# Optimization experiments

Measured on AMD Instinct MI355X. Metric: run time of the kernel, lower is better.

The kernel has to match this reference:

```python
import jax, jax.numpy as jnp
import numpy as np

SHAPES = ((92, 160), (46, 80), (23, 40), (12, 20))  # multi-scale (H, W) per level
B, NQ, C, M, P = 8, 900, 256, 8, 4
L = len(SHAPES)
D = C // M          # head dim = 32
S = sum(h * w for h, w in SHAPES)  # 19560 flattened keys
NC = 10
FFN = 1024


def setup_inputs() -> dict:
    key = jax.random.key(0)
    ks = jax.random.split(key, 16)
    f = lambda k, sh, s=0.02: jax.random.normal(k, sh, dtype=jnp.float32) * s
    return dict(
        query=jax.random.normal(ks[0], (B, NQ, C), dtype=jnp.float32),
        value=jax.random.normal(ks[1], (B, S, C), dtype=jnp.float32),
        ref_points=jax.random.uniform(ks[2], (B, NQ, 2), dtype=jnp.float32),
        w_value=f(ks[3], (C, C)), b_value=jnp.zeros((C,), jnp.float32),
        w_off=f(ks[4], (C, M * L * P * 2)), b_off=f(ks[5], (M * L * P * 2,), 0.5),
        w_attn=f(ks[6], (C, M * L * P)), b_attn=jnp.zeros((M * L * P,), jnp.float32),
        w_out=f(ks[7], (C, C)), b_out=jnp.zeros((C,), jnp.float32),
        ln1_w=jnp.ones((C,), jnp.float32), ln1_b=jnp.zeros((C,), jnp.float32),
        w_ffn1=f(ks[8], (C, FFN)), b_ffn1=jnp.zeros((FFN,), jnp.float32),
        w_ffn2=f(ks[9], (FFN, C)), b_ffn2=jnp.zeros((C,), jnp.float32),
        ln2_w=jnp.ones((C,), jnp.float32), ln2_b=jnp.zeros((C,), jnp.float32),
        w_cls=f(ks[10], (C, NC)), b_cls=jnp.zeros((NC,), jnp.float32),
    )


def _ln(x, w, b, eps=1e-6):
    u = x.mean(-1, keepdims=True)
    s = ((x - u) ** 2).mean(-1, keepdims=True)
    return (x - u) * jax.lax.rsqrt(s + eps) * w + b


def _sample_level(v_l, loc, Hl, Wl):
    # v_l: [B, Hl*Wl, M, D] level features; loc: [B, NQ, M, P, 2] normalized sampling locations.
    # Bilinear interpolation with zero padding (grid_sample align_corners=False convention).
    x = loc[..., 0] * Wl - 0.5
    y = loc[..., 1] * Hl - 0.5
    x0 = jnp.floor(x)
    y0 = jnp.floor(y)
    lx, ly = x - x0, y - y0
    vt = jnp.transpose(v_l, (0, 2, 1, 3))  # [B, M, S_l, D]

    def gather(xi, yi):
        valid = ((xi >= 0) & (xi < Wl) & (yi >= 0) & (yi < Hl)).astype(v_l.dtype)
        idx = (jnp.clip(yi, 0, Hl - 1) * Wl + jnp.clip(xi, 0, Wl - 1)).astype(jnp.int32)
        idx = jnp.transpose(idx, (0, 2, 1, 3)).reshape(B, M, NQ * P)
        g = jnp.take_along_axis(vt, idx[..., None], axis=2).reshape(B, M, NQ, P, D)
        return g * jnp.transpose(valid, (0, 2, 1, 3))[..., None]

    x0i, y0i = x0.astype(jnp.int32), y0.astype(jnp.int32)
    g00 = gather(x0i, y0i)
    g01 = gather(x0i + 1, y0i)
    g10 = gather(x0i, y0i + 1)
    g11 = gather(x0i + 1, y0i + 1)
    wx = jnp.transpose(lx, (0, 2, 1, 3))[..., None]
    wy = jnp.transpose(ly, (0, 2, 1, 3))[..., None]
    return g00 * (1 - wx) * (1 - wy) + g01 * wx * (1 - wy) + g10 * (1 - wx) * wy + g11 * wx * wy


def reference(query, value, ref_points, w_value, b_value, w_off, b_off, w_attn, b_attn,
              w_out, b_out, ln1_w, ln1_b, w_ffn1, b_ffn1, w_ffn2, b_ffn2, ln2_w, ln2_b,
              w_cls, b_cls):
    v = (value @ w_value + b_value).reshape(B, S, M, D)
    off = (query @ w_off + b_off).reshape(B, NQ, M, L, P, 2)
    attn = jax.nn.softmax((query @ w_attn + b_attn).reshape(B, NQ, M, L * P), axis=-1)
    attn = attn.reshape(B, NQ, M, L, P)
    norm = jnp.asarray([[w, h] for h, w in SHAPES], dtype=query.dtype)  # [L, 2] (W, H)
    loc = ref_points[:, :, None, None, None, :] + off / norm[None, None, None, :, None, :]

    out = jnp.zeros((B, M, NQ, D), dtype=query.dtype)
    start = 0
    for l, (Hl, Wl) in enumerate(SHAPES):
        v_l = jax.lax.dynamic_slice_in_dim(v, start, Hl * Wl, axis=1)
        samp = _sample_level(v_l, loc[:, :, :, l], Hl, Wl)          # [B, M, NQ, P, D]
        a = jnp.transpose(attn[:, :, :, l], (0, 2, 1, 3))[..., None]  # [B, M, NQ, P, 1]
        out = out + (samp * a).sum(3)
        start += Hl * Wl

    feat = jnp.transpose(out, (0, 2, 1, 3)).reshape(B, NQ, C) @ w_out + b_out
    x = _ln(query + feat, ln1_w, ln1_b)
    h = jax.nn.relu(x @ w_ffn1 + b_ffn1) @ w_ffn2 + b_ffn2
    x = _ln(x + h, ln2_w, ln2_b)
    return x @ w_cls + b_cls
```

## Files before the change

### kernel.cpp

```cpp
#include <hip/hip_runtime.h>
#include <cstddef>
#include <cstdint>

#define B_    8
#define NQ_   900
#define C_    256
#define M_    8
#define P_    4
#define L_    4
#define D_    32
#define S_    19560
#define NC_   10
#define FFN_  1024
#define RQ_   (B_ * NQ_)
#define RV_   (B_ * S_)

typedef __attribute__((ext_vector_type(8))) short bf8_t;
typedef __attribute__((ext_vector_type(8))) unsigned short us8_t;
typedef __attribute__((ext_vector_type(4))) float f4_t;
typedef unsigned short ushort_t;

__device__ __forceinline__ unsigned short f2bf(float x) {
    union { float f; unsigned u; } v; v.f = x;
    unsigned r = v.u + 0x7FFF + ((v.u >> 16) & 1);
    return (unsigned short)(r >> 16);
}
__device__ __forceinline__ float bfu2f(unsigned short u) {
    union { unsigned u; float f; } v; v.u = ((unsigned)u) << 16; return v.f;
}

__global__ __launch_bounds__(256) void prep_weights(
    const float* __restrict__ w_value, const float* __restrict__ w_off,
    const float* __restrict__ w_attn,  const float* __restrict__ w_out,
    const float* __restrict__ w_ffn1,  const float* __restrict__ w_ffn2,
    short* __restrict__ WvT, short* __restrict__ WoaT, short* __restrict__ WoutT,
    short* __restrict__ Wf1T, short* __restrict__ Wf2T)
{
    const int mat = blockIdx.z;
    int K, N; const float* src; short* dst;
    switch (mat) {
        case 0: K = 256;  N = 256;  src = w_value; dst = WvT;  break;
        case 1: K = 256;  N = 384;  src = nullptr; dst = WoaT; break;
        case 2: K = 256;  N = 256;  src = w_out;   dst = WoutT; break;
        case 3: K = 256;  N = 1024; src = w_ffn1;  dst = Wf1T; break;
        default:K = 1024; N = 256;  src = w_ffn2;  dst = Wf2T; break;
    }
    const int ntn = N >> 6;
    const int kt = blockIdx.x / ntn, nt = blockIdx.x % ntn;
    if (kt >= (K >> 6)) return;

    __shared__ float t[64][65];
    const int tx = threadIdx.x & 63;
    const int ty = threadIdx.x >> 6;
#pragma unroll
    for (int i = 0; i < 64; i += 4) {
        const int k = kt * 64 + i + ty;
        const int n = nt * 64 + tx;
        float v;
        if (mat == 1) v = (n < 256) ? w_off[(size_t)k * 256 + n]
                                    : w_attn[(size_t)k * 128 + (n - 256)];
        else          v = src[(size_t)k * N + n];
        t[i + ty][tx] = v;
    }
    __syncthreads();
#pragma unroll
    for (int i = 0; i < 64; i += 4) {
        const int n = nt * 64 + i + ty;
        const int k = kt * 64 + tx;
        dst[(size_t)n * K + k] = (short)f2bf(t[tx][i + ty]);
    }
}

__global__ __launch_bounds__(384) void prep_bias(
    const float* __restrict__ b_off, const float* __restrict__ b_attn,
    float* __restrict__ bias_cat)
{
    const int t = threadIdx.x;
    bias_cat[t] = (t < 256) ? b_off[t] : b_attn[t - 256];
}

template <int MODE, int BM>
__global__ __launch_bounds__(256) void gemm_mfma(
    const float* __restrict__ A, const short* __restrict__ WT,
    const float* __restrict__ bias, const float* __restrict__ res,
    float* __restrict__ out, int R, int N, int K)
{
    constexpr int NI  = BM / 32;
    constexpr int AIT = BM * 8 / 256;
    constexpr int ASB = BM * 128;
    constexpr int SMEM_BYTES = (MODE == 1) ? (128 * 136 * 2) : (ASB + 16384);

    __shared__ __align__(16) char smem[SMEM_BYTES];
    short* As = (short*)smem;
    short* Bs = (short*)(smem + ASB);

    const int tid  = threadIdx.x;
    const int lane = tid & 63;
    const int wave = tid >> 6;
    const int wr   = wave >> 1;
    const int wc   = wave & 1;
    const int g    = lane >> 4;
    const int fr   = lane & 15;

    const int row0 = blockIdx.x * BM;
    const int col0 = blockIdx.y * 128;

    const int r_base = tid >> 3;
    const int ku     = tid & 7;

    float4 rA[AIT][2];
#pragma unroll
    for (int it = 0; it < AIT; ++it) {
        rA[it][0] = make_float4(0.f, 0.f, 0.f, 0.f);
        rA[it][1] = make_float4(0.f, 0.f, 0.f, 0.f);
    }
    int4 rB[4];

    f4_t acc[NI][4] = {};

    auto LOAD = [&](int k0) {
#pragma unroll
        for (int it = 0; it < AIT; ++it) {
            const int grow = row0 + it * 32 + r_base;
            if (grow < R) {
                rA[it][0] = *(const float4*)(A + (size_t)grow * K + k0 + ku * 8);
                rA[it][1] = *(const float4*)(A + (size_t)grow * K + k0 + ku * 8 + 4);
            }
        }
#pragma unroll
        for (int it = 0; it < 4; ++it) {
            const int n = it * 32 + r_base;
            rB[it] = *(const int4*)(WT + (size_t)(col0 + n) * K + k0 + ku * 8);
        }
    };
    auto WRITE = [&]() {
#pragma unroll
        for (int it = 0; it < AIT; ++it) {
            const int r = it * 32 + r_base;
            const float va[8] = {rA[it][0].x, rA[it][0].y, rA[it][0].z, rA[it][0].w,
                                 rA[it][1].x, rA[it][1].y, rA[it][1].z, rA[it][1].w};
            bf8_t pk;
#pragma unroll
            for (int j = 0; j < 8; ++j) pk[j] = (short)f2bf(va[j]);
            *(bf8_t*)&As[r * 64 + (ku ^ (r & 7)) * 8] = pk;
        }
#pragma unroll
        for (int it = 0; it < 4; ++it) {
            const int n = it * 32 + r_base;
            *(int4*)&Bs[n * 64 + (ku ^ (n & 7)) * 8] = rB[it];
        }
    };

    LOAD(0);
    for (int k0 = 0; k0 < K; k0 += 64) {
        WRITE();
        __syncthreads();
        if (k0 + 64 < K) LOAD(k0 + 64);
#pragma unroll
        for (int c = 0; c < 2; ++c) {
            bf8_t fa[NI], fb[4];
#pragma unroll
            for (int i = 0; i < NI; ++i) {
                const int ar = wr * (BM / 2) + i * 16 + fr;
                fa[i] = *(const bf8_t*)&As[ar * 64 + ((c * 4 + g) ^ (ar & 7)) * 8];
            }
#pragma unroll
            for (int j = 0; j < 4; ++j) {
                const int br = wc * 64 + j * 16 + fr;
                fb[j] = *(const bf8_t*)&Bs[br * 64 + ((c * 4 + g) ^ (br & 7)) * 8];
            }
#pragma unroll
            for (int i = 0; i < NI; ++i)
#pragma unroll
                for (int j = 0; j < 4; ++j)
                    acc[i][j] = __builtin_amdgcn_mfma_f32_16x16x32_bf16(
                        fa[i], fb[j], acc[i][j], 0, 0, 0);
        }
        __syncthreads();
    }

    if (MODE == 1) {
        ushort_t* eps = (ushort_t*)smem;
        ushort_t* outv = (ushort_t*)out;
#pragma unroll
        for (int j = 0; j < 4; ++j) {
            const int col_l = wc * 64 + j * 16 + fr;
            const float bcol = bias[col0 + col_l];
#pragma unroll
            for (int i = 0; i < NI; ++i)
#pragma unroll
                for (int r = 0; r < 4; ++r) {
                    const int row_l = wr * 64 + i * 16 + g * 4 + r;
                    eps[row_l * 136 + col_l] = f2bf(acc[i][j][r] + bcol);
                }
        }
        __syncthreads();
#pragma unroll
        for (int u = 0; u < 8; ++u) {
            const int unit = u * 256 + tid;
            const int sl = unit >> 4;
            const int cc = unit & 15;
            const int grow = row0 + sl;
            if (grow < R) {
                const int b = grow / S_;
                const int s = grow - b * S_;
                const int col = col0 + cc * 8;
                const int m = col >> 5;
                const int d = col & 31;
                const int4 w = *(const int4*)&eps[sl * 136 + cc * 8];
                *(int4*)&outv[(((size_t)(b * M_ + m)) * S_ + s) * D_ + d] = w;
            }
        }
    } else {
#pragma unroll
        for (int j = 0; j < 4; ++j) {
            const int col = col0 + wc * 64 + j * 16 + fr;
            const float bcol = bias[col];
#pragma unroll
            for (int i = 0; i < NI; ++i) {
#pragma unroll
                for (int r = 0; r < 4; ++r) {
                    const int row = row0 + wr * (BM / 2) + i * 16 + g * 4 + r;
                    if (row >= R) continue;
                    float vv = acc[i][j][r] + bcol;
                    if (MODE == 2) {
                        out[(size_t)row * N + col] = fmaxf(vv, 0.f);
                    } else if (MODE == 3) {
                        out[(size_t)row * N + col] = vv + res[(size_t)row * N + col];
                    } else {
                        out[(size_t)row * N + col] = vv;
                    }
                }
            }
        }
    }
}

__global__ __launch_bounds__(128) void softmax_loc_kernel(
    const float* __restrict__ oa, const float* __restrict__ ref,
    float* __restrict__ loc, float* __restrict__ attn)
{
    const int row = blockIdx.x;
    const int t   = threadIdx.x;
    const float Wtab[L_] = {160.f, 80.f, 40.f, 20.f};
    const float Htab[L_] = {92.f, 46.f, 23.f, 12.f};

    float vlog = oa[(size_t)row * 384 + 256 + t];
    float mx = vlog;
#pragma unroll
    for (int o = 8; o >= 1; o >>= 1) mx = fmaxf(mx, __shfl_xor(mx, o, 64));
    const float e = __expf(vlog - mx);
    float sm = e;
#pragma unroll
    for (int o = 8; o >= 1; o >>= 1) sm += __shfl_xor(sm, o, 64);
    attn[(size_t)row * 128 + t] = e / sm;

    const int m = t >> 4, l = (t >> 2) & 3, p = t & 3;
    const float rx = ref[(size_t)row * 2 + 0];
    const float ry = ref[(size_t)row * 2 + 1];
    const int oi = m * 32 + l * 8 + p * 2;
    loc[(size_t)row * 256 + oi + 0] = rx * Wtab[l] + oa[(size_t)row * 384 + oi + 0] - 0.5f;
    loc[(size_t)row * 256 + oi + 1] = ry * Htab[l] + oa[(size_t)row * 384 + oi + 1] - 0.5f;
}

__global__ __launch_bounds__(256) void sample_kernel(
    const ushort_t* __restrict__ v, const float* __restrict__ loc,
    const float* __restrict__ attn, float* __restrict__ outf)
{
    const int row0 = blockIdx.x * 8;
    const int t    = threadIdx.x;
    const int rl   = t >> 5;
    const int m    = (t >> 2) & 7;
    const int dg   = t & 3;

    __shared__ float sloc[8][8][33];
    __shared__ float satt[8][8][17];

    {
        const float4* src = (const float4*)(loc + (size_t)row0 * 256);
#pragma unroll
        for (int i = 0; i < 2; ++i) {
            const int u   = i * 256 + t;
            const int r_  = u >> 6;
            const int rem = u & 63;
            const int m_  = rem >> 3;
            const int c4  = (rem & 7) * 4;
            *(float4*)&sloc[r_][m_][c4] = src[u];
        }
        const float4* asrc = (const float4*)(attn + (size_t)row0 * 128);
        {
            const int u   = t;
            const int r_  = u >> 5;
            const int rem = u & 31;
            const int m_  = rem >> 2;
            const int c4  = (rem & 3) * 4;
            *(float4*)&satt[r_][m_][c4] = asrc[u];
        }
    }
    __syncthreads();

    const int row = row0 + rl;
    const int b   = row / NQ_;
    const ushort_t* vbase = v + (((size_t)(b * M_ + m)) * S_) * D_ + dg * 8;

    const int Wtab[L_] = {160, 80, 40, 20};
    const int Htab[L_] = {92, 46, 23, 12};
    const int Stab[L_] = {0, 14720, 18400, 19320};

    float acc[8] = {};

#pragma unroll
    for (int l = 0; l < L_; ++l) {
        const int Wl = Wtab[l], Hl = Htab[l], st = Stab[l];
#pragma unroll
        for (int p = 0; p < P_; ++p) {
            const float x = sloc[rl][m][l * 8 + p * 2 + 0];
            const float y = sloc[rl][m][l * 8 + p * 2 + 1];
            const float a = satt[rl][m][l * 4 + p];
            const float xf = floorf(x), yf = floorf(y);
            const int x0 = (int)xf, y0 = (int)yf;
            const float lx = x - xf, ly = y - yf;
            const float wx0 = (x0 >= 0 && x0 < Wl)         ? (1.f - lx) : 0.f;
            const float wx1 = (x0 + 1 >= 0 && x0 + 1 < Wl) ? lx         : 0.f;
            const float wy0 = (y0 >= 0 && y0 < Hl)         ? (1.f - ly) : 0.f;
            const float wy1 = (y0 + 1 >= 0 && y0 + 1 < Hl) ? ly         : 0.f;
            const float ay0 = a * wy0, ay1 = a * wy1;
            const float aw00 = ay0 * wx0, aw01 = ay0 * wx1;
            const float aw10 = ay1 * wx0, aw11 = ay1 * wx1;
            const int xc0 = min(max(x0, 0), Wl - 1);
            const int xc1 = min(max(x0 + 1, 0), Wl - 1);
            const int yc0 = min(max(y0, 0), Hl - 1);
            const int yc1 = min(max(y0 + 1, 0), Hl - 1);
            const us8_t s00 = *(const us8_t*)(vbase + (size_t)(st + yc0 * Wl + xc0) * D_);
            const us8_t s01 = *(const us8_t*)(vbase + (size_t)(st + yc0 * Wl + xc1) * D_);
            const us8_t s10 = *(const us8_t*)(vbase + (size_t)(st + yc1 * Wl + xc0) * D_);
            const us8_t s11 = *(const us8_t*)(vbase + (size_t)(st + yc1 * Wl + xc1) * D_);
#pragma unroll
            for (int j = 0; j < 8; ++j)
                acc[j] += aw00 * bfu2f(s00[j]) + aw01 * bfu2f(s01[j])
                        + aw10 * bfu2f(s10[j]) + aw11 * bfu2f(s11[j]);
        }
    }

    float* o = outf + (size_t)row * 256 + m * 32 + dg * 8;
    *(float4*)o       = make_float4(acc[0], acc[1], acc[2], acc[3]);
    *((float4*)o + 1) = make_float4(acc[4], acc[5], acc[6], acc[7]);
}

__global__ __launch_bounds__(64) void ln_kernel(
    const float* __restrict__ in, const float* __restrict__ w,
    const float* __restrict__ bp, float* __restrict__ out)
{
    const int row  = blockIdx.x;
    const int lane = threadIdx.x;
    const float4 x = ((const float4*)(in + (size_t)row * C_))[lane];
    float s = x.x + x.y + x.z + x.w;
#pragma unroll
    for (int o = 32; o >= 1; o >>= 1) s += __shfl_xor(s, o, 64);
    const float mean = s * (1.f / C_);
    const float d0 = x.x - mean, d1 = x.y - mean, d2 = x.z - mean, d3 = x.w - mean;
    float ss = d0 * d0 + d1 * d1 + d2 * d2 + d3 * d3;
#pragma unroll
    for (int o = 32; o >= 1; o >>= 1) ss += __shfl_xor(ss, o, 64);
    const float r = rsqrtf(ss * (1.f / C_) + 1e-6f);
    const float4 wv = ((const float4*)w)[lane];
    const float4 bv = ((const float4*)bp)[lane];
    float4 o4;
    o4.x = d0 * r * wv.x + bv.x;
    o4.y = d1 * r * wv.y + bv.y;
    o4.z = d2 * r * wv.z + bv.z;
    o4.w = d3 * r * wv.w + bv.w;
    ((float4*)(out + (size_t)row * C_))[lane] = o4;
}

__global__ __launch_bounds__(64) void cls_kernel(
    const float* __restrict__ x, const float* __restrict__ w,
    const float* __restrict__ bias, float* __restrict__ out)
{
    const int row  = blockIdx.x;
    const int lane = threadIdx.x;
    float acc[NC_] = {};
#pragma unroll
    for (int j = 0; j < 4; ++j) {
        const int k = lane + j * 64;
        const float xk = x[(size_t)row * C_ + k];
        const float* wr = w + (size_t)k * NC_;
#pragma unroll
        for (int n = 0; n < NC_; ++n) acc[n] += xk * wr[n];
    }
#pragma unroll
    for (int n = 0; n < NC_; ++n) {
        float s = acc[n];
#pragma unroll
        for (int o = 32; o >= 1; o >>= 1) s += __shfl_xor(s, o, 64);
        if (lane == n) out[(size_t)row * NC_ + n] = s + bias[n];
    }
}

extern "C" void kernel_launch(void* const* d_in, const int* in_sizes, int n_in,
                              void* d_out, int out_size, void* d_ws, size_t ws_size,
                              hipStream_t stream)
{
    const float* query   = (const float*)d_in[0];
    const float* value   = (const float*)d_in[1];
    const float* refp    = (const float*)d_in[2];
    const float* w_value = (const float*)d_in[3];
    const float* b_value = (const float*)d_in[4];
    const float* w_off   = (const float*)d_in[5];
    const float* b_off   = (const float*)d_in[6];
    const float* w_attn  = (const float*)d_in[7];
    const float* b_attn  = (const float*)d_in[8];
    const float* w_out   = (const float*)d_in[9];
    const float* b_out   = (const float*)d_in[10];
    const float* ln1w    = (const float*)d_in[11];
    const float* ln1b    = (const float*)d_in[12];
    const float* w_ffn1  = (const float*)d_in[13];
    const float* b_ffn1  = (const float*)d_in[14];
    const float* w_ffn2  = (const float*)d_in[15];
    const float* b_ffn2  = (const float*)d_in[16];
    const float* ln2w    = (const float*)d_in[17];
    const float* ln2b    = (const float*)d_in[18];
    const float* w_cls   = (const float*)d_in[19];
    const float* b_cls   = (const float*)d_in[20];

    short* WvT   = (short*)d_ws;
    short* WoaT  = WvT  + 65536;
    short* WoutT = WoaT + 98304;
    short* Wf1T  = WoutT + 65536;
    short* Wf2T  = Wf1T + 262144;
    float* bias_cat = (float*)(Wf2T + 262144);
    ushort_t* v = (ushort_t*)(bias_cat + 384);
    float* oa   = (float*)(v + (size_t)RV_ * C_);
    float* loc  = oa   + (size_t)RQ_ * 384;
    float* attn = loc  + (size_t)RQ_ * 256;
    float* feat = attn + (size_t)RQ_ * 128;
    float* tmp  = feat + (size_t)RQ_ * 256;
    float* h    = tmp  + (size_t)RQ_ * 256;
    float* x2   = h    + (size_t)RQ_ * FFN_;

    prep_weights<<<dim3(64, 1, 5), 256, 0, stream>>>(
        w_value, w_off, w_attn, w_out, w_ffn1, w_ffn2,
        WvT, WoaT, WoutT, Wf1T, Wf2T);
    prep_bias<<<1, 384, 0, stream>>>(b_off, b_attn, bias_cat);

    gemm_mfma<1, 128><<<dim3((RV_ + 127) / 128, 2), 256, 0, stream>>>(
        value, WvT, b_value, nullptr, (float*)v, RV_, 256, 256);

    gemm_mfma<0, 64><<<dim3((RQ_ + 63) / 64, 3), 256, 0, stream>>>(
        query, WoaT, bias_cat, nullptr, oa, RQ_, 384, 256);

    softmax_loc_kernel<<<RQ_, 128, 0, stream>>>(oa, refp, loc, attn);

    sample_kernel<<<RQ_ / 8, 256, 0, stream>>>(v, loc, attn, feat);

    gemm_mfma<3, 64><<<dim3((RQ_ + 63) / 64, 2), 256, 0, stream>>>(
        feat, WoutT, b_out, query, tmp, RQ_, 256, 256);

    ln_kernel<<<RQ_, 64, 0, stream>>>(tmp, ln1w, ln1b, feat);

    gemm_mfma<2, 64><<<dim3((RQ_ + 63) / 64, 8), 256, 0, stream>>>(
        feat, Wf1T, b_ffn1, nullptr, h, RQ_, 1024, 256);

    gemm_mfma<3, 64><<<dim3((RQ_ + 63) / 64, 2), 256, 0, stream>>>(
        h, Wf2T, b_ffn2, feat, tmp, RQ_, 256, 1024);

    ln_kernel<<<RQ_, 64, 0, stream>>>(tmp, ln2w, ln2b, x2);

    cls_kernel<<<RQ_, 64, 0, stream>>>(x2, w_cls, b_cls, (float*)d_out);
}
```

Baseline: 504.8 us.

## Add dedicated full-width value projection GEMM with 512 threads per block

Result: faster. 493.6 us (-2.2%).

```diff
diff --git a/kernel.cpp b/kernel.cpp
--- a/kernel.cpp
+++ b/kernel.cpp
@@ -79,6 +79,135 @@
     bias_cat[t] = (t < 256) ? b_off[t] : b_attn[t - 256];
 }
 
+__global__ __launch_bounds__(512, 4) void gemm_value(
+    const float* __restrict__ A, const short* __restrict__ WT,
+    const float* __restrict__ bias, ushort_t* __restrict__ outv, int R)
+{
+    __shared__ __align__(16) char smem[49152];
+    short* As = (short*)smem;
+    short* Bs = (short*)(smem + 16384);
+
+    const int tid  = threadIdx.x;
+    const int lane = tid & 63;
+    const int wave = tid >> 6;
+    const int wr   = wave >> 2;
+    const int wc   = wave & 3;
+    const int g    = lane >> 4;
+    const int fr   = lane & 15;
+
+    const int row0 = blockIdx.x * 128;
+
+    const int r_base = tid >> 3;
+    const int ku     = tid & 7;
+
+    float4 rA[2][2];
+#pragma unroll
+    for (int it = 0; it < 2; ++it) {
+        rA[it][0] = make_float4(0.f, 0.f, 0.f, 0.f);
+        rA[it][1] = make_float4(0.f, 0.f, 0.f, 0.f);
+    }
+    int4 rB[4];
+    f4_t acc[4][4] = {};
+
+    auto LOAD = [&](int k0) {
+#pragma unroll
+        for (int it = 0; it < 2; ++it) {
+            const int grow = row0 + it * 64 + r_base;
+            if (grow < R) {
+                rA[it][0] = *(const float4*)(A + (size_t)grow * 256 + k0 + ku * 8);
+                rA[it][1] = *(const float4*)(A + (size_t)grow * 256 + k0 + ku * 8 + 4);
+            }
+        }
+#pragma unroll
+        for (int it = 0; it < 4; ++it) {
+            const int n = it * 64 + r_base;
+            rB[it] = *(const int4*)(WT + (size_t)n * 256 + k0 + ku * 8);
+        }
+    };
+    auto WRITE = [&]() {
+#pragma unroll
+        for (int it = 0; it < 2; ++it) {
+            const int r = it * 64 + r_base;
+            const float va[8] = {rA[it][0].x, rA[it][0].y, rA[it][0].z, rA[it][0].w,
+                                 rA[it][1].x, rA[it][1].y, rA[it][1].z, rA[it][1].w};
+            bf8_t pk;
+#pragma unroll
+            for (int j = 0; j < 8; ++j) pk[j] = (short)f2bf(va[j]);
+            *(bf8_t*)&As[r * 64 + (ku ^ (r & 7)) * 8] = pk;
+        }
+#pragma unroll
+        for (int it = 0; it < 4; ++it) {
+            const int n = it * 64 + r_base;
+            *(int4*)&Bs[n * 64 + (ku ^ (n & 7)) * 8] = rB[it];
+        }
+    };
+
+    LOAD(0);
+    for (int k0 = 0; k0 < 256; k0 += 64) {
+        WRITE();
+        __syncthreads();
+        if (k0 + 64 < 256) LOAD(k0 + 64);
+#pragma unroll
+        for (int c = 0; c < 2; ++c) {
+            bf8_t fa[4], fb[4];
+#pragma unroll
+            for (int i = 0; i < 4; ++i) {
+                const int ar = wr * 64 + i * 16 + fr;
+                fa[i] = *(const bf8_t*)&As[ar * 64 + ((c * 4 + g) ^ (ar & 7)) * 8];
+            }
+#pragma unroll
+            for (int j = 0; j < 4; ++j) {
+                const int br = wc * 64 + j * 16 + fr;
+                fb[j] = *(const bf8_t*)&Bs[br * 64 + ((c * 4 + g) ^ (br & 7)) * 8];
+            }
+#pragma unroll
+            for (int i = 0; i < 4; ++i)
+#pragma unroll
+                for (int j = 0; j < 4; ++j)
+                    acc[i][j] = __builtin_amdgcn_mfma_f32_16x16x32_bf16(
+                        fa[i], fb[j], acc[i][j], 0, 0, 0);
+        }
+        __syncthreads();
+    }
+
+    ushort_t* eps = (ushort_t*)smem;
+    for (int h = 0; h < 2; ++h) {
+        __syncthreads();
+        if ((wc >> 1) == h) {
+            const int wcl = wc & 1;
+#pragma unroll
+            for (int j = 0; j < 4; ++j) {
+                const int col_l = wcl * 64 + j * 16 + fr;
+                const float bcol = bias[h * 128 + col_l];
+#pragma unroll
+                for (int i = 0; i < 4; ++i)
+#pragma unroll
+                    for (int r = 0; r < 4; ++r) {
+                        const int row_l = wr * 64 + i * 16 + g * 4 + r;
+                        eps[row_l * 136 + col_l] = f2bf(acc[i][j][r] + bcol);
+                    }
+            }
+        }
+        __syncthreads();
+#pragma unroll
+        for (int u = 0; u < 4; ++u) {
+            const int unit = u * 512 + tid;
+            const int sl = unit >> 4;
+            const int cc = unit & 15;
+            const int grow = row0 + sl;
+            if (grow < R) {
+                const int b = grow / S_;
+                const int s = grow - b * S_;
+                const int col = h * 128 + cc * 8;
+                const int m = col >> 5;
+                const int d = col & 31;
+                *(int4*)&outv[(((size_t)(b * M_ + m)) * S_ + s) * D_ + d] =
+                    *(const int4*)&eps[sl * 136 + cc * 8];
+            }
+        }
+    }
+}
+
 template <int MODE, int BM>
 __global__ __launch_bounds__(256) void gemm_mfma(
     const float* __restrict__ A, const short* __restrict__ WT,
@@ -88,7 +217,7 @@
     constexpr int NI  = BM / 32;
     constexpr int AIT = BM * 8 / 256;
     constexpr int ASB = BM * 128;
-    constexpr int SMEM_BYTES = (MODE == 1) ? (128 * 136 * 2) : (ASB + 16384);
+    constexpr int SMEM_BYTES = ASB + 16384;
 
     __shared__ __align__(16) char smem[SMEM_BYTES];
     short* As = (short*)smem;
@@ -179,57 +308,23 @@
         __syncthreads();
     }
 
-    if (MODE == 1) {
-        ushort_t* eps = (ushort_t*)smem;
-        ushort_t* outv = (ushort_t*)out;
-#pragma unroll
-        for (int j = 0; j < 4; ++j) {
-            const int col_l = wc * 64 + j * 16 + fr;
-            const float bcol = bias[col0 + col_l];
-#pragma unroll
-            for (int i = 0; i < NI; ++i)
-#pragma unroll
-                for (int r = 0; r < 4; ++r) {
-                    const int row_l = wr * 64 + i * 16 + g * 4 + r;
-                    eps[row_l * 136 + col_l] = f2bf(acc[i][j][r] + bcol);
-                }
-        }
-        __syncthreads();
-#pragma unroll
-        for (int u = 0; u < 8; ++u) {
-            const int unit = u * 256 + tid;
-            const int sl = unit >> 4;
-            const int cc = unit & 15;
-            const int grow = row0 + sl;
-            if (grow < R) {
-                const int b = grow / S_;
-                const int s = grow - b * S_;
-                const int col = col0 + cc * 8;
-                const int m = col >> 5;
-                const int d = col & 31;
-                const int4 w = *(const int4*)&eps[sl * 136 + cc * 8];
-                *(int4*)&outv[(((size_t)(b * M_ + m)) * S_ + s) * D_ + d] = w;
-            }
-        }
-    } else {
-#pragma unroll
-        for (int j = 0; j < 4; ++j) {
-            const int col = col0 + wc * 64 + j * 16 + fr;
-            const float bcol = bias[col];
-#pragma unroll
-            for (int i = 0; i < NI; ++i) {
-#pragma unroll
-                for (int r = 0; r < 4; ++r) {
-                    const int row = row0 + wr * (BM / 2) + i * 16 + g * 4 + r;
-                    if (row >= R) continue;
-                    float vv = acc[i][j][r] + bcol;
-                    if (MODE == 2) {
-                        out[(size_t)row * N + col] = fmaxf(vv, 0.f);
-                    } else if (MODE == 3) {
-                        out[(size_t)row * N + col] = vv + res[(size_t)row * N + col];
-                    } else {
-                        out[(size_t)row * N + col] = vv;
-                    }
+#pragma unroll
+    for (int j = 0; j < 4; ++j) {
+        const int col = col0 + wc * 64 + j * 16 + fr;
+        const float bcol = bias[col];
+#pragma unroll
+        for (int i = 0; i < NI; ++i) {
+#pragma unroll
+            for (int r = 0; r < 4; ++r) {
+                const int row = row0 + wr * (BM / 2) + i * 16 + g * 4 + r;
+                if (row >= R) continue;
+                float vv = acc[i][j][r] + bcol;
+                if (MODE == 2) {
+                    out[(size_t)row * N + col] = fmaxf(vv, 0.f);
+                } else if (MODE == 3) {
+                    out[(size_t)row * N + col] = vv + res[(size_t)row * N + col];
+                } else {
+                    out[(size_t)row * N + col] = vv;
                 }
             }
         }
@@ -443,8 +538,8 @@
         WvT, WoaT, WoutT, Wf1T, Wf2T);
     prep_bias<<<1, 384, 0, stream>>>(b_off, b_attn, bias_cat);
 
-    gemm_mfma<1, 128><<<dim3((RV_ + 127) / 128, 2), 256, 0, stream>>>(
-        value, WvT, b_value, nullptr, (float*)v, RV_, 256, 256);
+    gemm_value<<<(RV_ + 127) / 128, 512, 0, stream>>>(
+        value, WvT, b_value, v, RV_);
 
     gemm_mfma<0, 64><<<dim3((RQ_ + 63) / 64, 3), 256, 0, stream>>>(
         query, WoaT, bias_cat, nullptr, oa, RQ_, 384, 256);
```
